# Optimization experiments

Measured on AMD Instinct MI355X. Metric: run time of the kernel, lower is better.

The kernel has to match this reference:

```python
import jax, jax.numpy as jnp
import numpy as np

N_NODES = 10000
T = 8
F_IN = 4
H1 = 16
HEADS = 4
H2 = 32
G = 32
PW = 16
E = 160000


def _gat(x, src, dst, W, a_src, a_dst, b, concat):
    # x: [T, N, Fin]; PyG GATConv (eval mode, dropout inactive), self-loops already in src/dst
    t, n, _ = x.shape
    heads, c = a_src.shape
    z = (x @ W).reshape(t, n, heads, c)                      # [T,N,H,C]
    asrc = jnp.einsum('tnhc,hc->tnh', z, a_src)
    adst = jnp.einsum('tnhc,hc->tnh', z, a_dst)
    e = jax.nn.leaky_relu(asrc[:, src] + adst[:, dst], 0.2)   # [T,E,H]
    e = e.transpose(1, 0, 2)                                  # [E,T,H]
    m = jax.ops.segment_max(e, dst, num_segments=n)           # [N,T,H]
    ex = jnp.exp(e - m[dst])
    s = jax.ops.segment_sum(ex, dst, num_segments=n)
    att = ex / s[dst]                                         # [E,T,H] softmax over in-edges of dst
    msg = z.transpose(1, 0, 2, 3)[src] * att[..., None]       # [E,T,H,C]
    out = jax.ops.segment_sum(msg, dst, num_segments=n)       # [N,T,H,C]
    out = out.transpose(1, 0, 2, 3)                           # [T,N,H,C]
    out = out.reshape(t, n, heads * c) if concat else out.mean(axis=2)
    return out + b


def _forward(dynamic, cI, cR, N, I, R, edge_index, h0,
             W1, att_src1, att_dst1, b1, W2, att_src2, att_dst2, b2,
             W_ih, W_hh, b_ih, b_hh, Wi, bi, Wr, br, Ws, bs):
    Npop = N.squeeze()
    loops = jnp.arange(N_NODES, dtype=edge_index.dtype)
    src = jnp.concatenate([edge_index[0], loops])
    dst = jnp.concatenate([edge_index[1], loops])
    x = dynamic.transpose(1, 0, 2)                            # [T,N,F] all timesteps batched
    x = jax.nn.elu(_gat(x, src, dst, W1, att_src1, att_dst1, b1, True))
    x = jax.nn.elu(_gat(x, src, dst, W2, att_src2, att_dst2, b2, False))
    cur_h = x.mean(axis=1)                                    # [T,H2]

    def gru_step(h, xt):  # torch GRUCell: gates in (r,z,n) order
        gi = W_ih @ xt + b_ih
        gh = W_hh @ h + b_hh
        ir, iz, inn = jnp.split(gi, 3)
        hr, hz, hn = jnp.split(gh, 3)
        r = jax.nn.sigmoid(ir + hr)
        zg = jax.nn.sigmoid(iz + hz)
        ng = jnp.tanh(inn + r * hn)
        hnew = (1.0 - zg) * ng + zg * h
        return hnew, hnew

    h_final, hs = jax.lax.scan(gru_step, h0[0], cur_h)        # hs: [T,G]
    hc = jnp.concatenate([hs, cI[:, None], cR[:, None]], axis=1)  # [T,G+2]
    new_I = (hc @ Wi.T + bi)[None]                            # [1,T,PW]
    new_R = (hc @ Wr.T + br)[None]
    sir = hc @ Ws.T + bs                                      # [T,2]
    alpha = jax.nn.sigmoid(sir[:, 0])
    beta = jax.nn.sigmoid(sir[:, 1])

    def sir_step(carry, _):
        lI, lR = carry
        lS = Npop - lI - lR
        dI = alpha * lI * (lS / Npop) - beta * lI
        dR = beta * lI
        # original accumulates detached increments
        return (lI + jax.lax.stop_gradient(dI), lR + jax.lax.stop_gradient(dR)), (dI, dR)

    _, (dIs, dRs) = jax.lax.scan(sir_step, (I, R), None, length=PW)  # [PW,T]
    phy_I = dIs.T[None]                                       # [1,T,PW]
    phy_R = dRs.T[None]
    return new_I, new_R, phy_I, phy_R, h_final[None]


def setup_inputs() -> dict:
    key = jax.random.key(0)
    ks = jax.random.split(key, 20)
    rn = lambda k, s, sc=0.1: (jax.random.normal(k, s) * sc).astype(jnp.float32)
    return {
        'dynamic': jax.random.normal(ks[0], (N_NODES, T, F_IN), jnp.float32),
        'cI': jax.random.uniform(ks[1], (T,), jnp.float32),
        'cR': jax.random.uniform(ks[2], (T,), jnp.float32),
        'N': jnp.ones((1,), jnp.float32) * 1e6,
        'I': jax.random.uniform(ks[3], (T,), jnp.float32) * 1e4,
        'R': jax.random.uniform(ks[4], (T,), jnp.float32) * 1e4,
        'edge_index': jax.random.randint(ks[5], (2, E), 0, N_NODES, dtype=jnp.int32),
        'h0': rn(ks[6], (1, G)),
        'W1': rn(ks[7], (F_IN, HEADS * H1)),
        'att_src1': rn(ks[8], (HEADS, H1)),
        'att_dst1': rn(ks[9], (HEADS, H1)),
        'b1': jnp.zeros((HEADS * H1,), jnp.float32),
        'W2': rn(ks[10], (HEADS * H1, H2)),
        'att_src2': rn(ks[11], (1, H2)),
        'att_dst2': rn(ks[12], (1, H2)),
        'b2': jnp.zeros((H2,), jnp.float32),
        'W_ih': rn(ks[13], (3 * G, H2)),
        'W_hh': rn(ks[14], (3 * G, G)),
        'b_ih': jnp.zeros((3 * G,), jnp.float32),
        'b_hh': jnp.zeros((3 * G,), jnp.float32),
        'Wi': rn(ks[15], (PW, G + 2)),
        'bi': jnp.zeros((PW,), jnp.float32),
        'Wr': rn(ks[16], (PW, G + 2)),
        'br': jnp.zeros((PW,), jnp.float32),
        'Ws': rn(ks[17], (2, G + 2)),
        'bs': jnp.zeros((2,), jnp.float32),
    }


def reference(dynamic, cI, cR, N, I, R, edge_index, h0,
              W1, att_src1, att_dst1, b1, W2, att_src2, att_dst2, b2,
              W_ih, W_hh, b_ih, b_hh, Wi, bi, Wr, br, Ws, bs):
    return _forward(dynamic, cI, cR, N, I, R, edge_index, h0,
                    W1, att_src1, att_dst1, b1, W2, att_src2, att_dst2, b2,
                    W_ih, W_hh, b_ih, b_hh, Wi, bi, Wr, br, Ws, bs)
```

## Files before the change

kernel.cpp:

```cpp
#include <hip/hip_runtime.h>

#define N_NODES 10000
#define T_STEPS 8
#define F_IN 4
#define H1 16
#define HEADS 4
#define H2 32
#define G 32
#define PW 16
#define E_EDGES 160000
#define CAP 64
#define NREP 32

__device__ __forceinline__ float lrelu(float x) { return x > 0.f ? x : 0.2f * x; }
__device__ __forceinline__ float eluf(float x) { return x > 0.f ? x : (__expf(x) - 1.f); }
__device__ __forceinline__ float sigmoidf(float x) { return 1.f / (1.f + expf(-x)); }
__device__ __forceinline__ float g8sum(float v) {
    v += __shfl_xor(v, 8);
    v += __shfl_xor(v, 16);
    v += __shfl_xor(v, 32);
    return v;
}
__device__ __forceinline__ float bf2f(unsigned int u) {
    return __uint_as_float(u << 16);
}
__device__ __forceinline__ unsigned short f2bf(float f) {
    unsigned b = __float_as_uint(f);
    return (unsigned short)((b + 0x7FFFu + ((b >> 16) & 1u)) >> 16);
}

__global__ void __launch_bounds__(256) k_scatter(
        const int* __restrict__ ei, int* __restrict__ cnt, int* __restrict__ colsrc,
        float* __restrict__ part, const unsigned* __restrict__ poison) {
    const unsigned P = *poison;
    int idx = blockIdx.x * 256 + threadIdx.x;
    if (idx < NREP * 256) part[idx] = 0.f;
    if (idx >= E_EDGES) return;
    int src = ei[idx];
    int dst = ei[E_EDGES + idx];
    unsigned pos = (unsigned)atomicAdd(&cnt[dst], 1) - P;
    if (pos < CAP) colsrc[(dst << 6) + pos] = src;
}

__global__ void __launch_bounds__(256) k_l1_node(
        const int* __restrict__ cnt, const int* __restrict__ colsrc,
        const float4* __restrict__ dyn, const float* __restrict__ W1,
        const float* __restrict__ as1, const float* __restrict__ ad1,
        const float* __restrict__ b1, const float* __restrict__ W2,
        const float* __restrict__ as2, const float* __restrict__ ad2,
        unsigned short* __restrict__ z2g, float* __restrict__ asrc2,
        float* __restrict__ adst2, const unsigned* __restrict__ poison) {
    __shared__ float sVA[16], sVD[16];
    __shared__ float sW1[256], sB1[64], sW2[64 * 32];
    __shared__ float sAs2[32], sAd2[32];
    __shared__ float sRow[4][8 * 72];
    const unsigned P = *poison;
    int tid = threadIdx.x;
    int lane = tid & 63, wslot = tid >> 6;
    int n = blockIdx.x * 4 + wslot;
    int t = lane & 7, es = lane >> 3;
    int beg = n << 6;
    unsigned dreal = (unsigned)cnt[n] - P; if (dreal > 63) dreal = 63;
    int deg = (int)dreal + 1;
    const float4 xo = dyn[(n << 3) + t];
    int srcs[8];
#pragma unroll
    for (int k = 0; k < 8; ++k) {
        int e = k * 8 + es;
        srcs[k] = (e < deg - 1) ? colsrc[beg + e] : n;
    }
    {
        const float4* W2v = (const float4*)W2;
        float4* sW2v = (float4*)sW2;
#pragma unroll
        for (int i = tid; i < 512; i += 256) sW2v[i] = W2v[i];
    }
    sW1[tid] = W1[tid];
    if (tid < 64) sB1[tid] = b1[tid];
    if (tid < 32) { sAs2[tid] = as2[tid]; sAd2[tid] = ad2[tid]; }
    if (tid < 32) {
        int q = tid & 15, d = q >> 2, hh = q & 3;
        const float* a = (tid < 16) ? as1 : ad1;
        float acc = 0.f;
#pragma unroll
        for (int c = 0; c < 16; ++c) acc += W1[d * 64 + hh * 16 + c] * a[hh * 16 + c];
        if (tid < 16) sVA[q] = acc;
        else sVD[q] = acc;
    }
    __syncthreads();

    float ad0 = xo.x * sVD[0] + xo.y * sVD[4] + xo.z * sVD[8]  + xo.w * sVD[12];
    float ad1v = xo.x * sVD[1] + xo.y * sVD[5] + xo.z * sVD[9]  + xo.w * sVD[13];
    float ad2v = xo.x * sVD[2] + xo.y * sVD[6] + xo.z * sVD[10] + xo.w * sVD[14];
    float ad3v = xo.x * sVD[3] + xo.y * sVD[7] + xo.z * sVD[11] + xo.w * sVD[15];

    float s0 = 0.f, s1 = 0.f, s2 = 0.f, s3 = 0.f;
    float u[16];
#pragma unroll
    for (int i = 0; i < 16; ++i) u[i] = 0.f;

    int kIters = (deg + 7) >> 3;
    for (int k = 0; k < kIters; ++k) {
        int e = k * 8 + es;
        bool act = e < deg;
        int src = srcs[k];
        const float4 x4 = dyn[(src << 3) + t];
        float l0 = x4.x * sVA[0] + x4.y * sVA[4] + x4.z * sVA[8]  + x4.w * sVA[12] + ad0;
        float l1 = x4.x * sVA[1] + x4.y * sVA[5] + x4.z * sVA[9]  + x4.w * sVA[13] + ad1v;
        float l2 = x4.x * sVA[2] + x4.y * sVA[6] + x4.z * sVA[10] + x4.w * sVA[14] + ad2v;
        float l3 = x4.x * sVA[3] + x4.y * sVA[7] + x4.z * sVA[11] + x4.w * sVA[15] + ad3v;
        float w0 = act ? __expf(lrelu(l0)) : 0.f;
        float w1 = act ? __expf(lrelu(l1)) : 0.f;
        float w2 = act ? __expf(lrelu(l2)) : 0.f;
        float w3 = act ? __expf(lrelu(l3)) : 0.f;
        s0 += w0; s1 += w1; s2 += w2; s3 += w3;
        u[0]  += w0 * x4.x; u[1]  += w0 * x4.y; u[2]  += w0 * x4.z; u[3]  += w0 * x4.w;
        u[4]  += w1 * x4.x; u[5]  += w1 * x4.y; u[6]  += w1 * x4.z; u[7]  += w1 * x4.w;
        u[8]  += w2 * x4.x; u[9]  += w2 * x4.y; u[10] += w2 * x4.z; u[11] += w2 * x4.w;
        u[12] += w3 * x4.x; u[13] += w3 * x4.y; u[14] += w3 * x4.z; u[15] += w3 * x4.w;
    }
    float red[20];
#pragma unroll
    for (int h2 = 0; h2 < 4; ++h2) {
        red[h2 * 5 + 0] = u[h2 * 4 + 0];
        red[h2 * 5 + 1] = u[h2 * 4 + 1];
        red[h2 * 5 + 2] = u[h2 * 4 + 2];
        red[h2 * 5 + 3] = u[h2 * 4 + 3];
    }
    red[4] = s0; red[9] = s1; red[14] = s2; red[19] = s3;
    bool lowHalf = (es < 4);
    float keep[10];
#pragma unroll
    for (int k = 0; k < 10; ++k) {
        float send = lowHalf ? red[10 + k] : red[k];
        float mine = lowHalf ? red[k] : red[10 + k];
        keep[k] = mine + __shfl_xor(send, 32);
    }
    bool firstPair = ((es & 2) == 0);
    float keep2[5];
#pragma unroll
    for (int k = 0; k < 5; ++k) {
        float send = firstPair ? keep[5 + k] : keep[k];
        float mine = firstPair ? keep[k] : keep[5 + k];
        keep2[k] = mine + __shfl_xor(send, 16);
    }
#pragma unroll
    for (int k = 0; k < 5; ++k) keep2[k] += __shfl_xor(keep2[k], 8);
    float uh0 = keep2[0], uh1 = keep2[1], uh2 = keep2[2], uh3 = keep2[3];
    float inv = 1.f / keep2[4];

    float4 ra, rb;
#pragma unroll
    for (int j = 0; j < 8; ++j) {
        int c = es * 8 + j;
        float acc = uh0 * sW1[c] + uh1 * sW1[64 + c] + uh2 * sW1[128 + c] + uh3 * sW1[192 + c];
        float v = eluf(acc * inv + sB1[c]);
        if (j < 4) ((float*)&ra)[j] = v;
        else ((float*)&rb)[j - 4] = v;
    }
    *reinterpret_cast<float4*>(&sRow[wslot][t * 72 + es * 8]) = ra;
    *reinterpret_cast<float4*>(&sRow[wslot][t * 72 + es * 8 + 4]) = rb;
    asm volatile("s_waitcnt lgkmcnt(0)" ::: "memory");
    float z0 = 0.f, z1v = 0.f, z2v = 0.f, z3v = 0.f;
#pragma unroll
    for (int j = 0; j < 64; j += 4) {
        float4 r4 = *reinterpret_cast<const float4*>(&sRow[wslot][t * 72 + j]);
        const float4 w0 = *reinterpret_cast<const float4*>(&sW2[(j + 0) * 32 + es * 4]);
        const float4 w1 = *reinterpret_cast<const float4*>(&sW2[(j + 1) * 32 + es * 4]);
        const float4 w2 = *reinterpret_cast<const float4*>(&sW2[(j + 2) * 32 + es * 4]);
        const float4 w3 = *reinterpret_cast<const float4*>(&sW2[(j + 3) * 32 + es * 4]);
        z0  += r4.x * w0.x + r4.y * w1.x + r4.z * w2.x + r4.w * w3.x;
        z1v += r4.x * w0.y + r4.y * w1.y + r4.z * w2.y + r4.w * w3.y;
        z2v += r4.x * w0.z + r4.y * w1.z + r4.z * w2.z + r4.w * w3.z;
        z3v += r4.x * w0.w + r4.y * w1.w + r4.z * w2.w + r4.w * w3.w;
    }
    int wid8 = (n << 3) + t;
    unsigned int p0 = (unsigned)f2bf(z0) | ((unsigned)f2bf(z1v) << 16);
    unsigned int p1 = (unsigned)f2bf(z2v) | ((unsigned)f2bf(z3v) << 16);
    *reinterpret_cast<uint2*>(z2g + (size_t)wid8 * 32 + es * 4) = make_uint2(p0, p1);
    float pa = z0 * sAs2[es * 4] + z1v * sAs2[es * 4 + 1] + z2v * sAs2[es * 4 + 2] + z3v * sAs2[es * 4 + 3];
    float pd = z0 * sAd2[es * 4] + z1v * sAd2[es * 4 + 1] + z2v * sAd2[es * 4 + 2] + z3v * sAd2[es * 4 + 3];
    pa = g8sum(pa);
    pd = g8sum(pd);
    if (es == 0) { asrc2[wid8] = pa; adst2[wid8] = pd; }
}

__global__ void __launch_bounds__(256) k_l2_node(
        const int* __restrict__ cnt, const int* __restrict__ colsrc,
        const float* __restrict__ asrc, const float* __restrict__ adst,
        const unsigned short* __restrict__ z2, const float* __restrict__ b2,
        float* __restrict__ part, const unsigned* __restrict__ poison) {
    __shared__ int sSrc[4][64];
    __shared__ float sW[4][64 * 8];
    __shared__ float sS[4][8];
    __shared__ float sB2[32];
    __shared__ float sPart[256];
    const unsigned P = *poison;
    int tid = threadIdx.x;
    int lane = tid & 63, wslot = tid >> 6;
    int n = blockIdx.x * 4 + wslot;
    int t = lane & 7, es = lane >> 3;
    int beg = n << 6;
    unsigned dreal = (unsigned)cnt[n] - P; if (dreal > 63) dreal = 63;
    int deg = (int)dreal + 1;
    float ad = adst[(n << 3) + t];
    int srcs2[8];
#pragma unroll
    for (int r = 0; r < 8; ++r) {
        int e = r * 8 + es;
        srcs2[r] = (e < deg - 1) ? colsrc[beg + e] : n;
    }
    if (tid < 32) sB2[tid] = b2[tid];
    sPart[tid] = 0.f;
    __syncthreads();

    int R = (deg + 7) >> 3;
    float ws = 0.f;
#pragma unroll
    for (int r = 0; r < 8; ++r) {
        if (r < R) {
            int e = r * 8 + es;
            int src = srcs2[r];
            float w = (e < deg) ? __expf(lrelu(asrc[(src << 3) + t] + ad)) : 0.f;
            ws += w;
            sW[wslot][e * 8 + t] = w;
            if (t == 0) sSrc[wslot][e] = src;
        }
    }
    float s = g8sum(ws);
    if (es == 0) sS[wslot][t] = s;
    asm volatile("s_waitcnt lgkmcnt(0)" ::: "memory");

    int eo = lane >> 5;
    int t2 = (lane >> 2) & 7;
    int cg4 = lane & 3;
    const unsigned short* zb = z2 + t2 * 32 + cg4 * 8;
    float a[8];
#pragma unroll
    for (int k = 0; k < 8; ++k) a[k] = 0.f;
    int iters = (deg + 1) >> 1;
    for (int i = 0; i < iters; ++i) {
        int e = 2 * i + eo;
        bool act = e < deg;
        int ee = act ? e : 0;
        int src = sSrc[wslot][ee];
        float w = act ? sW[wslot][ee * 8 + t2] : 0.f;
        uint4 pz = *reinterpret_cast<const uint4*>(zb + (size_t)src * 256);
        a[0] += w * bf2f(pz.x & 0xFFFFu);
        a[1] += w * bf2f(pz.x >> 16);
        a[2] += w * bf2f(pz.y & 0xFFFFu);
        a[3] += w * bf2f(pz.y >> 16);
        a[4] += w * bf2f(pz.z & 0xFFFFu);
        a[5] += w * bf2f(pz.z >> 16);
        a[6] += w * bf2f(pz.w & 0xFFFFu);
        a[7] += w * bf2f(pz.w >> 16);
    }
#pragma unroll
    for (int k = 0; k < 8; ++k) a[k] += __shfl_xor(a[k], 32);
    float invs = 1.f / sS[wslot][t2];
    int cbase = cg4 * 8 + eo * 4;
    int koff = eo * 4;
    int pidx = t2 * 32 + cbase;
    atomicAdd(&sPart[pidx],     eluf(a[koff]     * invs + sB2[cbase]));
    atomicAdd(&sPart[pidx + 1], eluf(a[koff + 1] * invs + sB2[cbase + 1]));
    atomicAdd(&sPart[pidx + 2], eluf(a[koff + 2] * invs + sB2[cbase + 2]));
    atomicAdd(&sPart[pidx + 3], eluf(a[koff + 3] * invs + sB2[cbase + 3]));
    __syncthreads();
    atomicAdd(&part[((blockIdx.x & (NREP - 1)) << 8) + tid], sPart[tid]);
}

__global__ void k_head(const float* __restrict__ part, const float* __restrict__ h0,
                       const float* __restrict__ W_ih, const float* __restrict__ W_hh,
                       const float* __restrict__ b_ih, const float* __restrict__ b_hh,
                       const float* __restrict__ Wi, const float* __restrict__ bi,
                       const float* __restrict__ Wr, const float* __restrict__ br,
                       const float* __restrict__ Ws, const float* __restrict__ bs,
                       const float* __restrict__ cI, const float* __restrict__ cR,
                       const float* __restrict__ Nptr, const float* __restrict__ Ivec,
                       const float* __restrict__ Rvec, float* __restrict__ out) {
    __shared__ float xs[256];
    __shared__ float h[32], gi[96], gh[96], hnew[32], hs[T_STEPS * 32], sirv[16];
    const float invN = 1.0f / (float)N_NODES;
    int j = threadIdx.x;
    {
        float sx = 0.f, sy = 0.f;
        const float2* p2 = (const float2*)part;
        for (int r = 0; r < NREP; ++r) {
            float2 v = p2[r * 128 + j];
            sx += v.x; sy += v.y;
        }
        xs[2 * j] = sx * invN;
        xs[2 * j + 1] = sy * invN;
    }
    if (j < 32) h[j] = h0[j];
    __syncthreads();
    for (int t = 0; t < T_STEPS; ++t) {
        if (j < 96) {
            float accI = b_ih[j], accH = b_hh[j];
            for (int k = 0; k < 32; ++k) {
                accI += W_ih[j * 32 + k] * xs[t * 32 + k];
                accH += W_hh[j * 32 + k] * h[k];
            }
            gi[j] = accI;
            gh[j] = accH;
        }
        __syncthreads();
        if (j < 32) {
            float r = sigmoidf(gi[j] + gh[j]);
            float zg = sigmoidf(gi[32 + j] + gh[32 + j]);
            float ng = tanhf(gi[64 + j] + r * gh[64 + j]);
            hnew[j] = (1.f - zg) * ng + zg * h[j];
        }
        __syncthreads();
        if (j < 32) {
            h[j] = hnew[j];
            hs[t * 32 + j] = hnew[j];
        }
        __syncthreads();
    }
    if (j < 32) out[512 + j] = h[j];
    {
        int t = j >> 4, p = j & 15;
        float accI = bi[p], accR = br[p];
        for (int k = 0; k < 34; ++k) {
            float hck = (k < 32) ? hs[t * 32 + k] : (k == 32 ? cI[t] : cR[t]);
            accI += hck * Wi[p * 34 + k];
            accR += hck * Wr[p * 34 + k];
        }
        out[j] = accI;
        out[128 + j] = accR;
    }
    if (j < 16) {
        int t = j >> 1, q = j & 1;
        float acc = bs[q];
        for (int k = 0; k < 34; ++k) {
            float hck = (k < 32) ? hs[t * 32 + k] : (k == 32 ? cI[t] : cR[t]);
            acc += hck * Ws[q * 34 + k];
        }
        sirv[j] = acc;
    }
    __syncthreads();
    if (j < 8) {
        int t = j;
        float alpha = sigmoidf(sirv[2 * t]);
        float beta = sigmoidf(sirv[2 * t + 1]);
        float Np = Nptr[0];
        float lI = Ivec[t], lR = Rvec[t];
        for (int p = 0; p < PW; ++p) {
            float lS = Np - lI - lR;
            float dI = alpha * lI * (lS / Np) - beta * lI;
            float dR = beta * lI;
            out[256 + t * 16 + p] = dI;
            out[384 + t * 16 + p] = dR;
            lI += dI;
            lR += dR;
        }
    }
}

extern "C" void kernel_launch(void* const* d_in, const int* in_sizes, int n_in,
                              void* d_out, int out_size, void* d_ws, size_t ws_size,
                              hipStream_t stream) {
    const float* dyn = (const float*)d_in[0];
    const float* cI = (const float*)d_in[1];
    const float* cR = (const float*)d_in[2];
    const float* Nptr = (const float*)d_in[3];
    const float* Ivec = (const float*)d_in[4];
    const float* Rvec = (const float*)d_in[5];
    const int* ei = (const int*)d_in[6];
    const float* h0 = (const float*)d_in[7];
    const float* W1 = (const float*)d_in[8];
    const float* as1 = (const float*)d_in[9];
    const float* ad1 = (const float*)d_in[10];
    const float* b1 = (const float*)d_in[11];
    const float* W2 = (const float*)d_in[12];
    const float* as2 = (const float*)d_in[13];
    const float* ad2 = (const float*)d_in[14];
    const float* b2 = (const float*)d_in[15];
    const float* W_ih = (const float*)d_in[16];
    const float* W_hh = (const float*)d_in[17];
    const float* b_ih = (const float*)d_in[18];
    const float* b_hh = (const float*)d_in[19];
    const float* Wi = (const float*)d_in[20];
    const float* bi = (const float*)d_in[21];
    const float* Wr = (const float*)d_in[22];
    const float* br = (const float*)d_in[23];
    const float* Ws = (const float*)d_in[24];
    const float* bs = (const float*)d_in[25];
    float* out = (float*)d_out;

    char* ws = (char*)d_ws;
    size_t off = 0;
    auto alloc = [&](size_t bytes) {
        void* p = ws + off;
        off += (bytes + 255) & ~(size_t)255;
        return p;
    };
    const size_t TN = (size_t)T_STEPS * N_NODES;
    int* cnt = (int*)alloc(N_NODES * 4);
    float* part = (float*)alloc((size_t)NREP * 256 * 4);
    unsigned short* z2 = (unsigned short*)alloc(TN * 32 * 2);
    float* asrc2 = (float*)alloc(TN * 4);
    float* adst2 = (float*)alloc(TN * 4);
    int* colsrc = (int*)alloc((size_t)N_NODES * CAP * 4);
    unsigned* poison = (unsigned*)alloc(4);
    (void)ws_size; (void)in_sizes; (void)n_in; (void)out_size;

    const int BT = 256;
    int gEdge = (E_EDGES + BT - 1) / BT;
    k_scatter<<<gEdge, BT, 0, stream>>>(ei, cnt, colsrc, part, poison);
    k_l1_node<<<N_NODES / 4, BT, 0, stream>>>(cnt, colsrc, (const float4*)dyn,
                                              W1, as1, ad1, b1, W2, as2, ad2,
                                              z2, asrc2, adst2, poison);
    k_l2_node<<<N_NODES / 4, BT, 0, stream>>>(cnt, colsrc, asrc2, adst2, z2, b2, part, poison);
    k_head<<<1, 128, 0, stream>>>(part, h0, W_ih, W_hh, b_ih, b_hh, Wi, bi, Wr, br, Ws, bs,
                                  cI, cR, Nptr, Ivec, Rvec, out);
}
```

Measured before the change: 172.9 us.

## Prefetch neighbor gathers before barriers and vectorize edge scatter to pairs

The edge scatter kernel now processes two edges per thread with int2 loads and clears the partial buffer with float4 stores. The layer-1 and layer-2 node kernels issue all neighbor gathers (node features and source attention logits) into registers up front, before the shared-memory setup and barrier, so memory latency overlaps with setup work. The aggregation loops are unrolled. This raises register pressure and does unconditional loads for padded slots (self index), which wastes some bandwidth on low-degree nodes.

Result: no change. 175.5 us (+1.5%).

```diff
diff --git a/kernel.cpp b/kernel.cpp
--- a/kernel.cpp
+++ b/kernel.cpp
@@ -33,13 +33,15 @@
         const int* __restrict__ ei, int* __restrict__ cnt, int* __restrict__ colsrc,
         float* __restrict__ part, const unsigned* __restrict__ poison) {
     const unsigned P = *poison;
-    int idx = blockIdx.x * 256 + threadIdx.x;
-    if (idx < NREP * 256) part[idx] = 0.f;
-    if (idx >= E_EDGES) return;
-    int src = ei[idx];
-    int dst = ei[E_EDGES + idx];
-    unsigned pos = (unsigned)atomicAdd(&cnt[dst], 1) - P;
-    if (pos < CAP) colsrc[(dst << 6) + pos] = src;
+    int idx2 = blockIdx.x * 256 + threadIdx.x;
+    if (idx2 < NREP * 64) ((float4*)part)[idx2] = make_float4(0.f, 0.f, 0.f, 0.f);
+    if (idx2 >= E_EDGES / 2) return;
+    int2 s2 = ((const int2*)ei)[idx2];
+    int2 d2 = ((const int2*)(ei + E_EDGES))[idx2];
+    unsigned pos0 = (unsigned)atomicAdd(&cnt[d2.x], 1) - P;
+    if (pos0 < CAP) colsrc[(d2.x << 6) + pos0] = s2.x;
+    unsigned pos1 = (unsigned)atomicAdd(&cnt[d2.y], 1) - P;
+    if (pos1 < CAP) colsrc[(d2.y << 6) + pos1] = s2.y;
 }
 
 __global__ void __launch_bounds__(256) k_l1_node(
@@ -69,6 +71,9 @@
         int e = k * 8 + es;
         srcs[k] = (e < deg - 1) ? colsrc[beg + e] : n;
     }
+    float4 x4r[8];
+#pragma unroll
+    for (int k = 0; k < 8; ++k) x4r[k] = dyn[(srcs[k] << 3) + t];
     {
         const float4* W2v = (const float4*)W2;
         float4* sW2v = (float4*)sW2;
@@ -100,11 +105,12 @@
     for (int i = 0; i < 16; ++i) u[i] = 0.f;
 
     int kIters = (deg + 7) >> 3;
-    for (int k = 0; k < kIters; ++k) {
+#pragma unroll
+    for (int k = 0; k < 8; ++k) {
+        if (k >= kIters) break;
         int e = k * 8 + es;
         bool act = e < deg;
-        int src = srcs[k];
-        const float4 x4 = dyn[(src << 3) + t];
+        const float4 x4 = x4r[k];
         float l0 = x4.x * sVA[0] + x4.y * sVA[4] + x4.z * sVA[8]  + x4.w * sVA[12] + ad0;
         float l1 = x4.x * sVA[1] + x4.y * sVA[5] + x4.z * sVA[9]  + x4.w * sVA[13] + ad1v;
         float l2 = x4.x * sVA[2] + x4.y * sVA[6] + x4.z * sVA[10] + x4.w * sVA[14] + ad2v;
@@ -210,22 +216,21 @@
         int e = r * 8 + es;
         srcs2[r] = (e < deg - 1) ? colsrc[beg + e] : n;
     }
+    float avr[8];
+#pragma unroll
+    for (int r = 0; r < 8; ++r) avr[r] = asrc[(srcs2[r] << 3) + t];
     if (tid < 32) sB2[tid] = b2[tid];
     sPart[tid] = 0.f;
     __syncthreads();
 
-    int R = (deg + 7) >> 3;
     float ws = 0.f;
 #pragma unroll
     for (int r = 0; r < 8; ++r) {
-        if (r < R) {
-            int e = r * 8 + es;
-            int src = srcs2[r];
-            float w = (e < deg) ? __expf(lrelu(asrc[(src << 3) + t] + ad)) : 0.f;
-            ws += w;
-            sW[wslot][e * 8 + t] = w;
-            if (t == 0) sSrc[wslot][e] = src;
-        }
+        int e = r * 8 + es;
+        float w = (e < deg) ? __expf(lrelu(avr[r] + ad)) : 0.f;
+        ws += w;
+        sW[wslot][e * 8 + t] = w;
+        if (t == 0) sSrc[wslot][e] = srcs2[r];
     }
     float s = g8sum(ws);
     if (es == 0) sS[wslot][t] = s;
@@ -239,6 +244,7 @@
 #pragma unroll
     for (int k = 0; k < 8; ++k) a[k] = 0.f;
     int iters = (deg + 1) >> 1;
+#pragma unroll 4
     for (int i = 0; i < iters; ++i) {
         int e = 2 * i + eo;
         bool act = e < deg;
@@ -407,8 +413,8 @@
     (void)ws_size; (void)in_sizes; (void)n_in; (void)out_size;
 
     const int BT = 256;
-    int gEdge = (E_EDGES + BT - 1) / BT;
-    k_scatter<<<gEdge, BT, 0, stream>>>(ei, cnt, colsrc, part, poison);
+    int gPair = (E_EDGES / 2 + BT - 1) / BT;
+    k_scatter<<<gPair, BT, 0, stream>>>(ei, cnt, colsrc, part, poison);
     k_l1_node<<<N_NODES / 4, BT, 0, stream>>>(cnt, colsrc, (const float4*)dyn,
                                               W1, as1, ad1, b1, W2, as2, ad2,
                                               z2, asrc2, adst2, poison);
```
